# Kernel tuning notes

Measured on AMD Instinct MI355X. Metric: run time of the kernel, lower is better.

The kernel has to match this reference:

```python
import jax, jax.numpy as jnp
import numpy as np

GAMMAS = (0.01, 0.1, 1.0, 10.0, 100.0)
FOCAL_GAMMA = 2.0
SMOOTH = 0.1
TASK_W = (0.4, 0.3, 0.3)
A_RECON, A_ORTH, A_ADV = 1.0, 0.1, 0.1
NUM_DOMAINS = 4
NUM_LABELS1 = 4


def focal_smooth(logits, targets, maskf):
    # FocalLoss.forward with smoothing > 0, masked mean
    n_classes = logits.shape[1]
    log_p = jax.nn.log_softmax(logits, axis=1)
    p = jnp.exp(log_p)
    onehot = jax.nn.one_hot(targets, n_classes, dtype=logits.dtype)
    smooth = onehot * (1.0 - SMOOTH) + SMOOTH / n_classes
    ce = -(smooth * log_p).sum(axis=1)
    pt = jnp.take_along_axis(p, targets[:, None], axis=1)[:, 0]
    loss = ce * (1.0 - pt) ** FOCAL_GAMMA
    return (loss * maskf).sum() / jnp.maximum(maskf.sum(), 1.0)


def ce_masked(logits, targets, maskf):
    log_p = jax.nn.log_softmax(logits, axis=1)
    nll = -jnp.take_along_axis(log_p, targets[:, None], axis=1)[:, 0]
    return (nll * maskf).sum() / jnp.maximum(maskf.sum(), 1.0)


def cond_mmd(feats, domains, labels, maskf):
    # Global pairwise sq-distance matrix; multi-gamma RBF kernels summed.
    sq = (feats ** 2).sum(axis=-1)                      # (B,)
    Dmat = sq[:, None] + sq[None, :] - 2.0 * feats @ feats.T  # (B,B)
    Ksum = jnp.zeros_like(Dmat)
    for g in GAMMAS:
        Ksum = Ksum + jnp.exp(-g * Dmat)
    loss = jnp.asarray(0.0, feats.dtype)
    count = jnp.asarray(0.0, feats.dtype)
    for lab in range(NUM_LABELS1):
        lm = (labels == lab).astype(feats.dtype) * maskf
        for d1 in range(NUM_DOMAINS):
            m1 = lm * (domains == d1).astype(feats.dtype)
            n1 = m1.sum()
            Km1 = Ksum @ m1
            for d2 in range(d1 + 1, NUM_DOMAINS):
                m2 = lm * (domains == d2).astype(feats.dtype)
                n2 = m2.sum()
                valid = (n1 > 1) & (n2 > 1)
                term = (m1 @ Km1) / jnp.maximum(n1, 1.0) ** 2 \
                     + (m2 @ (Ksum @ m2)) / jnp.maximum(n2, 1.0) ** 2 \
                     - 2.0 * (m2 @ Km1) / jnp.maximum(n1 * n2, 1.0)
                loss = loss + jnp.where(valid, term, 0.0)
                count = count + valid.astype(feats.dtype)
    return loss / jnp.maximum(count, 1.0)


def hsic(c, s):
    n = c.shape[0]
    c = c / jnp.maximum(jnp.linalg.norm(c, axis=-1, keepdims=True), 1e-12)
    s = s / jnp.maximum(jnp.linalg.norm(s, axis=-1, keepdims=True), 1e-12)
    K = c @ c.T
    L = s @ s.T
    Kc = K - K.mean(axis=0, keepdims=True) - K.mean(axis=1, keepdims=True) + K.mean()
    Lc = L - L.mean(axis=0, keepdims=True) - L.mean(axis=1, keepdims=True) + L.mean()
    return (Kc * Lc).sum() / (n - 1) ** 2


def setup_inputs() -> dict:
    key = jax.random.key(0)
    ks = jax.random.split(key, 20)
    B, D, H = 4096, 256, 768
    inp = {
        'logits1': jax.random.normal(ks[0], (B, 4), jnp.float32),
        'labels1': jax.random.randint(ks[1], (B,), 0, 4),
        'logits2': jax.random.normal(ks[2], (B, 6), jnp.float32),
        'labels2': jax.random.randint(ks[3], (B,), 0, 6),
        'logits3': jax.random.normal(ks[4], (B, 3), jnp.float32),
        'labels3': jax.random.randint(ks[5], (B,), 0, 3),
        'c_v': jax.random.normal(ks[6], (B, D), jnp.float32),
        's_v': jax.random.normal(ks[7], (B, D), jnp.float32),
        'c_t': jax.random.normal(ks[8], (B, D), jnp.float32),
        's_t': jax.random.normal(ks[9], (B, D), jnp.float32),
        'v_sv': jax.random.normal(ks[10], (B, NUM_DOMAINS), jnp.float32),
        'v_st': jax.random.normal(ks[11], (B, NUM_DOMAINS), jnp.float32),
        'domain_labels': jax.random.randint(ks[12], (B,), 0, NUM_DOMAINS),
        'mask': jnp.ones((B,), dtype=bool),
        'h_img_recon': jax.random.normal(ks[13], (B, H), jnp.float32),
        'h_img_orig': jax.random.normal(ks[14], (B, H), jnp.float32),
        'h_txt_recon': jax.random.normal(ks[15], (B, H), jnp.float32),
        'h_txt_orig': jax.random.normal(ks[16], (B, H), jnp.float32),
    }
    return inp


def reference(logits1, labels1, logits2, labels2, logits3, labels3,
              c_v, s_v, c_t, s_t, v_sv, v_st, domain_labels, mask,
              h_img_recon, h_img_orig, h_txt_recon, h_txt_orig):
    maskf = mask.astype(jnp.float32)
    total = jnp.asarray(0.0, jnp.float32)
    # classification (focal + label smoothing), per-task weighted
    total = total + TASK_W[0] * focal_smooth(logits1, labels1, maskf)
    total = total + TASK_W[1] * focal_smooth(logits2, labels2, maskf)
    total = total + TASK_W[2] * focal_smooth(logits3, labels3, maskf)
    # adversarial: CE on spurious domain logits + conditional MMD on causal feats
    l_adv_s = ce_masked(v_sv, domain_labels, maskf) + ce_masked(v_st, domain_labels, maskf)
    l_adv_c = cond_mmd(c_v, domain_labels, labels1, maskf) \
            + cond_mmd(c_t, domain_labels, labels1, maskf)
    total = total + A_ADV * (l_adv_s + l_adv_c)
    # orthogonality (HSIC), on unmasked features as in source
    l_orth = hsic(c_v, s_v) + hsic(c_t, s_t)
    total = total + A_ORTH * l_orth
    # reconstruction MSE
    l_recon = jnp.mean((h_img_recon - h_img_orig) ** 2) + jnp.mean((h_txt_recon - h_txt_orig) ** 2)
    total = total + A_RECON * l_recon
    return total
```

## Files before the change

### kernel.cpp

```cpp
#include <hip/hip_runtime.h>
#include <hip/hip_bf16.h>


typedef short bf16x8 __attribute__((ext_vector_type(8)));
typedef float f32x4 __attribute__((ext_vector_type(4)));
typedef unsigned long long u64;
typedef unsigned int u32;

static constexpr int D = 256;
static constexpr int H = 768;
static constexpr int NG = 16;
static constexpr float FX32 = 4294967296.f;
static constexpr float IFX32 = 2.3283064365386963e-10f;

__device__ inline void gAddFx(u64* p, float v) {
  long long q = (long long)llroundf(v * FX32);
  atomicAdd(p, (u64)q);
}
__device__ inline float fxToF(u64 v) { return (float)(long long)v * IFX32; }

__device__ inline float focal_n(const float* x, int n, int tgt,
                                float s_over_n, float oms) {
  float mx = x[0];
  for (int c = 1; c < n; ++c) mx = fmaxf(mx, x[c]);
  float se = 0.f, sx = 0.f;
  for (int c = 0; c < n; ++c) { se += __expf(x[c] - mx); sx += x[c]; }
  float logZ = mx + __logf(se);
  float ce = logZ - oms * x[tgt] - s_over_n * sx;
  float pt = __expf(x[tgt] - logZ);
  float om = 1.f - pt;
  return ce * om * om;
}

extern "C" __global__ __launch_bounds__(256) void k_pre(
    const void* __restrict__ mask, const int* __restrict__ y1,
    const int* __restrict__ dom,
    const float* __restrict__ l1, const float* __restrict__ l2,
    const float* __restrict__ l3, const int* __restrict__ y2,
    const int* __restrict__ y3,
    const float* __restrict__ vsv, const float* __restrict__ vst,
    const float* __restrict__ cv, const float* __restrict__ sv,
    const float* __restrict__ ct, const float* __restrict__ st,
    const float* __restrict__ ir, const float* __restrict__ io,
    const float* __restrict__ trc, const float* __restrict__ to,
    u64* SA, u64* GCU, u64* U64,
    int* gid, float* sq, float* inv, unsigned short* bf,
    int B, int N4, int NA, int NB) {
  __shared__ u32 sh3[3];
  __shared__ u32 cnt[NG];
  __shared__ int redi[4];
  __shared__ float redf[4];
  int bid = blockIdx.x;
  int t = threadIdx.x;

  if (bid < NA) {
    if (t < 3) sh3[t] = 0;
    if (t < NG) cnt[t] = 0;
    __syncthreads();
    u32 a = 0, b2 = 0, cd = 0;
    if (t * 16 + 15 < B) {
      uint4 wv = ((const uint4*)mask)[t];
      u32 ws[4] = {wv.x, wv.y, wv.z, wv.w};
      #pragma unroll
      for (int j = 0; j < 4; ++j) {
        a |= ws[j] & 0xffu; b2 |= ws[j] & 0xff00u; cd |= ws[j] & 0xffff0000u;
      }
    }
    if (a) atomicOr(&sh3[0], 1u);
    if (b2) atomicOr(&sh3[1], 1u);
    if (cd) atomicOr(&sh3[2], 1u);
    __syncthreads();
    int mode;
    if ((sh3[1] | sh3[2]) == 0) mode = 0;
    else if (sh3[0] == 0 && sh3[1] == 0) mode = 1;
    else mode = 2;
    int r = bid * 256 + t;
    int mi = 0;
    float s[5] = {0.f, 0.f, 0.f, 0.f, 0.f};
    if (r < B) {
      if (mode == 0)      mi = ((const int*)mask)[r] ? 1 : 0;
      else if (mode == 1) mi = (((const float*)mask)[r] != 0.f) ? 1 : 0;
      else                mi = ((const unsigned char*)mask)[r] ? 1 : 0;
      int g = -1;
      if (mi) { g = y1[r] * 4 + dom[r]; atomicAdd(&cnt[g], 1u); }
      gid[r] = g;
      if (mi) {
        float x[6];
        for (int c = 0; c < 4; ++c) x[c] = l1[r * 4 + c];
        s[0] = focal_n(x, 4, y1[r], 0.1f / 4.f, 0.9f);
        for (int c = 0; c < 6; ++c) x[c] = l2[r * 6 + c];
        s[1] = focal_n(x, 6, y2[r], 0.1f / 6.f, 0.9f);
        for (int c = 0; c < 3; ++c) x[c] = l3[r * 3 + c];
        s[2] = focal_n(x, 3, y3[r], 0.1f / 3.f, 0.9f);
        int d = dom[r];
        for (int c = 0; c < 4; ++c) x[c] = vsv[r * 4 + c];
        {
          float mx = fmaxf(fmaxf(x[0], x[1]), fmaxf(x[2], x[3]));
          float se = __expf(x[0]-mx)+__expf(x[1]-mx)+__expf(x[2]-mx)+__expf(x[3]-mx);
          s[3] = mx + __logf(se) - x[d];
        }
        for (int c = 0; c < 4; ++c) x[c] = vst[r * 4 + c];
        {
          float mx = fmaxf(fmaxf(x[0], x[1]), fmaxf(x[2], x[3]));
          float se = __expf(x[0]-mx)+__expf(x[1]-mx)+__expf(x[2]-mx)+__expf(x[3]-mx);
          s[4] = mx + __logf(se) - x[d];
        }
      }
    }
    int v = mi;
    #pragma unroll
    for (int o = 32; o > 0; o >>= 1) v += __shfl_down(v, o);
    if ((t & 63) == 0) redi[t >> 6] = v;
    __syncthreads();
    if (t == 0) atomicAdd(&SA[5], (u64)(redi[0] + redi[1] + redi[2] + redi[3]));
    if (t < NG && cnt[t]) atomicAdd(&GCU[t], (u64)cnt[t]);
    for (int k = 0; k < 5; ++k) {
      float x = s[k];
      #pragma unroll
      for (int o = 32; o > 0; o >>= 1) x += __shfl_down(x, o);
      __syncthreads();
      if ((t & 63) == 0) redf[t >> 6] = x;
      __syncthreads();
      if (t == 0) gAddFx(&SA[k], redf[0] + redf[1] + redf[2] + redf[3]);
    }
  } else if (bid < NA + NB) {
    int b = bid - NA;
    int f = b >> 6;
    int rb = b & 63;
    const float* p = (f == 0) ? cv : (f == 1) ? sv : (f == 2) ? ct : st;
    int w = t >> 6, L = t & 63;
    float up0 = 0.f, up1 = 0.f, up2 = 0.f, up3 = 0.f;
    for (int k = 0; k < 16; ++k) {
      int r = rb * 64 + w * 16 + k;
      float4 v = ((const float4*)(p + (size_t)r * D))[L];
      float ss = v.x * v.x + v.y * v.y + v.z * v.z + v.w * v.w;
      #pragma unroll
      for (int o = 32; o > 0; o >>= 1) ss += __shfl_down(ss, o);
      ss = __shfl(ss, 0);
      float iv = 1.f / fmaxf(sqrtf(ss), 1e-12f);
      if ((f & 1) == 0) {
        int fi = f >> 1;
        alignas(8) __hip_bfloat16 hb[4];
        hb[0] = __float2bfloat16(v.x); hb[1] = __float2bfloat16(v.y);
        hb[2] = __float2bfloat16(v.z); hb[3] = __float2bfloat16(v.w);
        *(uint2*)(bf + ((size_t)fi * B + r) * D + L * 4) = *(uint2*)hb;
        if (L == 0) sq[fi * B + r] = ss;
      }
      if (L == 0) inv[f * B + r] = iv;
      up0 += v.x * iv; up1 += v.y * iv; up2 += v.z * iv; up3 += v.w * iv;
    }
    u64* Uf = U64 + f * D + 4 * L;
    gAddFx(Uf + 0, up0); gAddFx(Uf + 1, up1);
    gAddFx(Uf + 2, up2); gAddFx(Uf + 3, up3);
  } else {
    int cidx = bid - (NA + NB);
    int j = cidx >> 8;
    int cb = cidx & 255;
    const float4* A  = (const float4*)(j ? trc : ir);
    const float4* Bp = (const float4*)(j ? to : io);
    float acc = 0.f;
    for (int idx = cb * 256 + t; idx < N4; idx += 256 * 256) {
      float4 a = A[idx], b = Bp[idx];
      float dx = a.x-b.x, dy = a.y-b.y, dz = a.z-b.z, dw = a.w-b.w;
      acc += dx*dx + dy*dy + dz*dz + dw*dw;
    }
    #pragma unroll
    for (int o = 32; o > 0; o >>= 1) acc += __shfl_down(acc, o);
    if ((t & 63) == 0) redf[t >> 6] = acc;
    __syncthreads();
    if (t == 0) gAddFx(&SA[6 + j], redf[0] + redf[1] + redf[2] + redf[3]);
  }
}

extern "C" __global__ __launch_bounds__(256) void k_big(
    const float* __restrict__ cv, const float* __restrict__ sv,
    const float* __restrict__ ct, const float* __restrict__ st,
    const float* __restrict__ inv, u64* M64,
    const unsigned short* __restrict__ bf, const float* __restrict__ sq,
    const int* __restrict__ gid, u64* GSP, int B) {
  __shared__ __align__(16) char smem[38016];
  int bid = blockIdx.x;
  int tid = threadIdx.x;

  if (bid < 512) {
    float (*lc)[16] = (float(*)[16])smem;
    float* lis = (float*)(smem + 16384);
    int p = bid >> 8;
    int a0 = ((bid >> 4) & 15) * 16;
    int i0 = (bid & 15) * 256;
    const float* c = p ? ct : cv;
    const float* s = p ? st : sv;
    const float* ic = inv + (2 * p) * B;
    const float* is = inv + (2 * p + 1) * B;
    int t = tid;
    if (t < 256) lis[t] = is[i0 + t];
    for (int e = t; e < 256 * 16; e += 256) {
      int i = e >> 4, rr = e & 15;
      lc[i][rr] = c[(size_t)(i0 + i) * D + a0 + rr] * ic[i0 + i];
    }
    __syncthreads();
    float4 acc[4];
    #pragma unroll
    for (int r = 0; r < 4; ++r) acc[r] = make_float4(0.f, 0.f, 0.f, 0.f);
    #pragma unroll 8
    for (int i = 0; i < 256; ++i) {
      float svv = s[(size_t)(i0 + i) * D + t] * lis[i];
      const float4* lr = (const float4*)lc[i];
      #pragma unroll
      for (int r = 0; r < 4; ++r) {
        float4 c4 = lr[r];
        acc[r].x += c4.x * svv; acc[r].y += c4.y * svv;
        acc[r].z += c4.z * svv; acc[r].w += c4.w * svv;
      }
    }
    u64* Mp = M64 + (size_t)p * D * D;
    #pragma unroll
    for (int r = 0; r < 4; ++r) {
      gAddFx(&Mp[(a0 + 4 * r + 0) * D + t], acc[r].x);
      gAddFx(&Mp[(a0 + 4 * r + 1) * D + t], acc[r].y);
      gAddFx(&Mp[(a0 + 4 * r + 2) * D + t], acc[r].z);
      gAddFx(&Mp[(a0 + 4 * r + 3) * D + t], acc[r].w);
    }
    return;
  }

  unsigned short* Ab = (unsigned short*)smem;
  unsigned short* Bb = (unsigned short*)(smem + 16384);
  u32 (*gsw)[264] = (u32(*)[264])(smem + 32768);
  int*   gA = (int*)(smem + 36992);
  int*   gB = gA + 64;
  float* sA = (float*)(gB + 64);
  float* sB = sA + 64;

  int idx2 = bid - 512;
  int feat = idx2 & 1;
  int tlin = idx2 >> 1;
  int NT = B / 64;
  float tf = (float)tlin;
  int ti = (int)((2.f * NT + 1.f -
                  sqrtf((2.f * NT + 1.f) * (2.f * NT + 1.f) - 8.f * tf)) * 0.5f);
  while (ti > 0 && (ti * NT - (ti * (ti - 1)) / 2) > tlin) --ti;
  while (((ti + 1) * NT - ((ti + 1) * ti) / 2) <= tlin) ++ti;
  int tj = ti + (tlin - (ti * NT - (ti * (ti - 1)) / 2));
  int i0 = ti * 64, j0 = tj * 64;
  bool diag = (ti == tj);
  const unsigned short* fb = bf + (size_t)feat * B * D;
  const float* sqf = sq + (size_t)feat * B;

  int w = tid >> 6, L = tid & 63, m = L & 15, q = L >> 4;

  {
    u32* gz = (u32*)gsw;
    for (int e = tid; e < 4 * 264; e += 256) gz[e] = 0;
    if (tid < 64) { gA[tid] = gid[i0 + tid]; sA[tid] = sqf[i0 + tid]; }
    else if (tid < 128) { int r = tid - 64; gB[r] = gid[j0 + r]; sB[r] = sqf[j0 + r]; }
  }

  f32x4 acc[4] = {{0.f,0.f,0.f,0.f},{0.f,0.f,0.f,0.f},{0.f,0.f,0.f,0.f},{0.f,0.f,0.f,0.f}};

  for (int h = 0; h < 2; ++h) {
    if (h) __syncthreads();
    for (int e = tid; e < 1024; e += 256) {
      int row = e >> 4, ck = e & 15;
      uint4 v = *(const uint4*)(fb + (size_t)(i0 + row) * D + h * 128 + ck * 8);
      *(uint4*)&Ab[row * 128 + ((ck ^ (row & 15)) * 8)] = v;
    }
    if (!diag) {
      for (int e = tid; e < 1024; e += 256) {
        int row = e >> 4, ck = e & 15;
        uint4 v = *(const uint4*)(fb + (size_t)(j0 + row) * D + h * 128 + ck * 8);
        *(uint4*)&Bb[row * 128 + ((ck ^ (row & 15)) * 8)] = v;
      }
    }
    __syncthreads();
    const unsigned short* Bp = diag ? Ab : Bb;
    #pragma unroll
    for (int kk = 0; kk < 4; ++kk) {
      int ar = w * 16 + m;
      bf16x8 aF = *(const bf16x8*)&Ab[ar * 128 + (((kk * 4 + q) ^ (ar & 15)) * 8)];
      #pragma unroll
      for (int c = 0; c < 4; ++c) {
        int br = c * 16 + m;
        bf16x8 bF = *(const bf16x8*)&Bp[br * 128 + (((kk * 4 + q) ^ (br & 15)) * 8)];
        acc[c] = __builtin_amdgcn_mfma_f32_16x16x32_bf16(aF, bF, acc[c], 0, 0, 0);
      }
    }
  }
  int ri0 = w * 16 + q * 4;
  int gi0 = gA[ri0], gi1 = gA[ri0+1], gi2 = gA[ri0+2], gi3 = gA[ri0+3];
  float si0 = sA[ri0], si1 = sA[ri0+1], si2 = sA[ri0+2], si3 = sA[ri0+3];
  int giv[4] = {gi0, gi1, gi2, gi3};
  float siv[4] = {si0, si1, si2, si3};
  #pragma unroll
  for (int c = 0; c < 4; ++c) {
    int rj = c * 16 + m;
    int gj = gB[rj];
    float sb = sB[rj];
    #pragma unroll
    for (int v = 0; v < 4; ++v) {
      int ri = ri0 + v;
      int gi = giv[v];
      if (gi >= 0 && gj >= 0 && !(diag && ri > rj)) {
        float K;
        if (diag && ri == rj) K = 5.f;
        else {
          float d = fmaxf(siv[v] + sb - 2.f * acc[c][v], 0.f);
          K = __expf(-0.01f * d) + __expf(-0.1f * d) + __expf(-d)
            + __expf(-10.f * d) + __expf(-100.f * d);
        }
        u32 kf = (u32)(K * 65536.f + 0.5f);
        int a = min(gi, gj), b = max(gi, gj);
        atomicAdd(&gsw[w][a * NG + b], kf);
      }
    }
  }
  __syncthreads();
  if (tid < NG * NG) {
    u64 s = (u64)gsw[0][tid] + gsw[1][tid] + gsw[2][tid] + gsw[3][tid];
    if (s)
      atomicAdd(&GSP[((size_t)(tlin & 63) * 2 + feat) * NG * NG + tid], s);
  }
}

extern "C" __global__ __launch_bounds__(256) void k_hsic(
    const u64* __restrict__ U64, const u64* __restrict__ M64, u64* SA) {
  __shared__ float red[8];
  __shared__ float ush[32], vsh[D];
  int p = blockIdx.y;
  int k0 = blockIdx.x * 32;
  int t = threadIdx.x;
  vsh[t] = fxToF(U64[(2 * p + 1) * D + t]);
  if (t < 32) ush[t] = fxToF(U64[(2 * p) * D + k0 + t]);
  __syncthreads();
  const u64* Mp = M64 + (size_t)p * D * D;
  float trkl = 0.f, cr = 0.f;
  #pragma unroll 4
  for (int k = 0; k < 32; ++k) {
    float mv = fxToF(Mp[(size_t)(k0 + k) * D + t]);
    trkl += mv * mv;
    cr += ush[k] * mv;
  }
  cr *= vsh[t];
  #pragma unroll
  for (int o = 32; o > 0; o >>= 1) { trkl += __shfl_down(trkl, o); cr += __shfl_down(cr, o); }
  if ((t & 63) == 0) { red[t >> 6] = trkl; red[4 + (t >> 6)] = cr; }
  __syncthreads();
  if (t == 0) gAddFx(&SA[10 + p], red[0] + red[1] + red[2] + red[3]);
  if (t == 64) gAddFx(&SA[12 + p], red[4] + red[5] + red[6] + red[7]);
}

extern "C" __global__ __launch_bounds__(256) void k_final(
    const u64* SA, const u64* GCU, const u64* GSP,
    const u64* U64, float* out, int B) {
  __shared__ float red[8];
  __shared__ float gssh[2 * NG * NG];
  int t = threadIdx.x;
  for (int e = t; e < 2 * NG * NG; e += 256) {
    u64 ssum = 0;
    int f = e >> 8, idx = e & 255;
    for (int cpy = 0; cpy < 64; ++cpy)
      ssum += GSP[((size_t)cpy * 2 + f) * NG * NG + idx];
    gssh[e] = (float)((double)ssum * (1.0 / 65536.0));
  }
  __syncthreads();

  float n = (float)B;
  float hs[2];
  for (int p = 0; p < 2; ++p) {
    float ut = fxToF(U64[(2 * p) * D + t]);
    float vt = fxToF(U64[(2 * p + 1) * D + t]);
    float uu = ut * ut, vv = vt * vt;
    #pragma unroll
    for (int o = 32; o > 0; o >>= 1) { uu += __shfl_down(uu, o); vv += __shfl_down(vv, o); }
    __syncthreads();
    if ((t & 63) == 0) { red[t >> 6] = uu; red[4 + (t >> 6)] = vv; }
    __syncthreads();
    float uus = red[0] + red[1] + red[2] + red[3];
    float vvs = red[4] + red[5] + red[6] + red[7];
    float trkl = (float)((double)(long long)SA[10 + p] * (double)IFX32);
    float cr   = (float)((double)(long long)SA[12 + p] * (double)IFX32);
    hs[p] = (trkl - (2.f / n) * cr + uus * vvs / (n * n))
          / ((n - 1.f) * (n - 1.f));
    __syncthreads();
  }
  if (t == 0) {
    float msum = fmaxf((float)SA[5], 1.f);
    float f1 = fxToF(SA[0]) / msum;
    float f2 = fxToF(SA[1]) / msum;
    float f3 = fxToF(SA[2]) / msum;
    float cesv = fxToF(SA[3]) / msum;
    float cest = fxToF(SA[4]) / msum;
    float mmd[2];
    for (int f = 0; f < 2; ++f) {
      float loss = 0.f, cntv = 0.f;
      for (int lab = 0; lab < 4; ++lab)
        for (int d1 = 0; d1 < 4; ++d1)
          for (int d2 = d1 + 1; d2 < 4; ++d2) {
            int a = lab * 4 + d1, b = lab * 4 + d2;
            float n1 = (float)GCU[a], n2 = (float)GCU[b];
            if (n1 > 1.f && n2 > 1.f) {
              float g11 = 2.f * gssh[f * 256 + a * NG + a] - 5.f * n1;
              float g22 = 2.f * gssh[f * 256 + b * NG + b] - 5.f * n2;
              float g12 = gssh[f * 256 + a * NG + b];
              loss += g11 / (fmaxf(n1, 1.f) * fmaxf(n1, 1.f))
                    + g22 / (fmaxf(n2, 1.f) * fmaxf(n2, 1.f))
                    - 2.f * g12 / fmaxf(n1 * n2, 1.f);
              cntv += 1.f;
            }
          }
      mmd[f] = loss / fmaxf(cntv, 1.f);
    }
    double rs = ((double)(long long)SA[6] + (double)(long long)SA[7])
              * (double)IFX32;
    float recon = (float)(rs / ((double)B * (double)H));
    float total = 0.4f * f1 + 0.3f * f2 + 0.3f * f3
                + 0.1f * (cesv + cest + mmd[0] + mmd[1])
                + 0.1f * (hs[0] + hs[1])
                + recon;
    out[0] = total;
  }
}

extern "C" void kernel_launch(void* const* d_in, const int* in_sizes, int n_in,
                              void* d_out, int out_size, void* d_ws, size_t ws_size,
                              hipStream_t stream) {
  const float* l1  = (const float*)d_in[0];
  const int*   y1  = (const int*)d_in[1];
  const float* l2  = (const float*)d_in[2];
  const int*   y2  = (const int*)d_in[3];
  const float* l3  = (const float*)d_in[4];
  const int*   y3  = (const int*)d_in[5];
  const float* cv  = (const float*)d_in[6];
  const float* sv  = (const float*)d_in[7];
  const float* ct  = (const float*)d_in[8];
  const float* st  = (const float*)d_in[9];
  const float* vsv = (const float*)d_in[10];
  const float* vst = (const float*)d_in[11];
  const int*   dom = (const int*)d_in[12];
  const void*  mask= d_in[13];
  const float* ir  = (const float*)d_in[14];
  const float* io  = (const float*)d_in[15];
  const float* trc = (const float*)d_in[16];
  const float* to  = (const float*)d_in[17];
  int B = in_sizes[1];

  u64* SA  = (u64*)d_ws;
  u64* GCU = SA + 32;
  u64* U64 = GCU + 16;
  u64* M64 = U64 + 4 * D;
  u64* GSP = M64 + 2 * D * D;
  u64* zend = GSP + 64 * 2 * NG * NG;
  size_t zeroBytes = (size_t)((char*)zend - (char*)d_ws);
  int*   gid = (int*)zend;
  float* sq  = (float*)(gid + B);
  float* inv = sq + 2 * B;
  unsigned short* bf = (unsigned short*)(inv + 4 * B);

  int NA = B / 256;
  int NB = 4 * (B / 64);
  int NC = 512;
  int N4 = B * H / 4;

  hipMemsetAsync(d_ws, 0, zeroBytes, stream);
  k_pre<<<NA + NB + NC, 256, 0, stream>>>(
      mask, y1, dom, l1, l2, l3, y2, y3, vsv, vst,
      cv, sv, ct, st, ir, io, trc, to,
      SA, GCU, U64, gid, sq, inv, bf, B, N4, NA, NB);
  int NT = B / 64;
  int nmmd = 2 * (NT * (NT + 1) / 2);
  k_big<<<512 + nmmd, 256, 0, stream>>>(cv, sv, ct, st, inv, M64,
                                        bf, sq, gid, GSP, B);
  k_hsic<<<dim3(8, 2), 256, 0, stream>>>(U64, M64, SA);
  k_final<<<1, 256, 0, stream>>>(SA, GCU, GSP, U64, (float*)d_out, B);
}
```

Measured before the change: 249.4 us.

## Sort rows by label-domain group to replace per-element LDS atomics in MMD tiles

Adds a counting-sort kernel that permutes samples by (label, domain) group, with masked rows placed last. The MMD tiles then gather rows through the permutation. Tiles made only of masked rows exit early, and tiles spanning at most two groups per axis reduce the kernel sums in registers with a wave shuffle and issue a few global atomics, instead of one shared-memory atomic per element. The K-loop is re-tiled to 64-wide chunks, which cuts shared memory and can raise occupancy. In exchange it adds a kernel launch, gathered (non-contiguous) row loads, and a slow fallback path with per-element global atomics for tiles that span many groups.

```diff
diff --git a/kernel.cpp b/kernel.cpp
--- a/kernel.cpp
+++ b/kernel.cpp
@@ -44,10 +44,10 @@
     const float* __restrict__ ir, const float* __restrict__ io,
     const float* __restrict__ trc, const float* __restrict__ to,
     u64* SA, u64* GCU, u64* U64,
-    int* gid, float* sq, float* inv, unsigned short* bf,
+    int* gid, float* sq, float* inv, unsigned short* bf, u32* CNTB,
     int B, int N4, int NA, int NB) {
   __shared__ u32 sh3[3];
-  __shared__ u32 cnt[NG];
+  __shared__ u32 cnt[17];
   __shared__ int redi[4];
   __shared__ float redf[4];
   int bid = blockIdx.x;
@@ -55,7 +55,7 @@
 
   if (bid < NA) {
     if (t < 3) sh3[t] = 0;
-    if (t < NG) cnt[t] = 0;
+    if (t < 17) cnt[t] = 0;
     __syncthreads();
     u32 a = 0, b2 = 0, cd = 0;
     if (t * 16 + 15 < B) {
@@ -83,6 +83,7 @@
       else                mi = ((const unsigned char*)mask)[r] ? 1 : 0;
       int g = -1;
       if (mi) { g = y1[r] * 4 + dom[r]; atomicAdd(&cnt[g], 1u); }
+      else atomicAdd(&cnt[16], 1u);
       gid[r] = g;
       if (mi) {
         float x[6];
@@ -114,6 +115,7 @@
     __syncthreads();
     if (t == 0) atomicAdd(&SA[5], (u64)(redi[0] + redi[1] + redi[2] + redi[3]));
     if (t < NG && cnt[t]) atomicAdd(&GCU[t], (u64)cnt[t]);
+    if (t < 17) CNTB[bid * 17 + t] = cnt[t];
     for (int k = 0; k < 5; ++k) {
       float x = s[k];
       #pragma unroll
@@ -172,13 +174,52 @@
   }
 }
 
+extern "C" __global__ __launch_bounds__(256) void k_sort(
+    const u32* __restrict__ CNTB, const int* __restrict__ gid,
+    const float* __restrict__ sq, int* __restrict__ perm,
+    float* __restrict__ sqp, int* __restrict__ OFF, int B, int NA) {
+  __shared__ int lg[256];
+  __shared__ u32 cbs[17], tots[17];
+  int b = blockIdx.x, t = threadIdx.x;
+  if (t < 17) {
+    u32 cb = 0, tot = 0;
+    for (int b2 = 0; b2 < NA; ++b2) {
+      u32 c = CNTB[b2 * 17 + t];
+      cb += (b2 < b) ? c : 0u;
+      tot += c;
+    }
+    cbs[t] = cb; tots[t] = tot;
+  }
+  int r = b * 256 + t;
+  int g = 16;
+  if (r < B) { int gg = gid[r]; g = (gg < 0) ? 16 : gg; }
+  lg[t] = g;
+  __syncthreads();
+  if (b == 0 && t < 18) {
+    u32 bb = 0;
+    for (int g2 = 0; g2 < t; ++g2) bb += tots[g2];
+    OFF[t] = (int)bb;
+  }
+  if (r < B) {
+    u32 base = 0;
+    for (int g2 = 0; g2 < g; ++g2) base += tots[g2];
+    int rank = 0;
+    for (int t2 = 0; t2 < t; ++t2) rank += (lg[t2] == g) ? 1 : 0;
+    int pos = (int)(base + cbs[g]) + rank;
+    perm[pos] = r;
+    sqp[pos] = sq[r];
+    sqp[B + pos] = sq[B + r];
+  }
+}
+
 extern "C" __global__ __launch_bounds__(256) void k_big(
     const float* __restrict__ cv, const float* __restrict__ sv,
     const float* __restrict__ ct, const float* __restrict__ st,
     const float* __restrict__ inv, u64* M64,
-    const unsigned short* __restrict__ bf, const float* __restrict__ sq,
-    const int* __restrict__ gid, u64* GSP, int B) {
-  __shared__ __align__(16) char smem[38016];
+    const unsigned short* __restrict__ bf, const float* __restrict__ sqp,
+    const int* __restrict__ perm, const int* __restrict__ OFF,
+    u64* GSP, int B) {
+  __shared__ __align__(16) char smem[17536];
   int bid = blockIdx.x;
   int tid = threadIdx.x;
 
@@ -225,12 +266,12 @@
   }
 
   unsigned short* Ab = (unsigned short*)smem;
-  unsigned short* Bb = (unsigned short*)(smem + 16384);
-  u32 (*gsw)[264] = (u32(*)[264])(smem + 32768);
-  int*   gA = (int*)(smem + 36992);
-  int*   gB = gA + 64;
-  float* sA = (float*)(gB + 64);
-  float* sB = sA + 64;
+  unsigned short* Bb = (unsigned short*)(smem + 8192);
+  float* sA = (float*)(smem + 16384);
+  float* sB = (float*)(smem + 16640);
+  int*   pA = (int*)(smem + 16896);
+  int*   pB = (int*)(smem + 17152);
+  int*   offs = (int*)(smem + 17408);
 
   int idx2 = bid - 512;
   int feat = idx2 & 1;
@@ -245,80 +286,146 @@
   int i0 = ti * 64, j0 = tj * 64;
   bool diag = (ti == tj);
   const unsigned short* fb = bf + (size_t)feat * B * D;
-  const float* sqf = sq + (size_t)feat * B;
+  const float* sqf = sqp + (size_t)feat * B;
 
   int w = tid >> 6, L = tid & 63, m = L & 15, q = L >> 4;
 
-  {
-    u32* gz = (u32*)gsw;
-    for (int e = tid; e < 4 * 264; e += 256) gz[e] = 0;
-    if (tid < 64) { gA[tid] = gid[i0 + tid]; sA[tid] = sqf[i0 + tid]; }
-    else if (tid < 128) { int r = tid - 64; gB[r] = gid[j0 + r]; sB[r] = sqf[j0 + r]; }
-  }
-
-  f32x4 acc[4] = {{0.f,0.f,0.f,0.f},{0.f,0.f,0.f,0.f},{0.f,0.f,0.f,0.f},{0.f,0.f,0.f,0.f}};
-
-  for (int h = 0; h < 2; ++h) {
-    if (h) __syncthreads();
-    for (int e = tid; e < 1024; e += 256) {
-      int row = e >> 4, ck = e & 15;
-      uint4 v = *(const uint4*)(fb + (size_t)(i0 + row) * D + h * 128 + ck * 8);
-      *(uint4*)&Ab[row * 128 + ((ck ^ (row & 15)) * 8)] = v;
+  if (tid < 64) { pA[tid] = perm[i0 + tid]; sA[tid] = sqf[i0 + tid]; }
+  else if (tid < 128) { int r = tid - 64; pB[r] = perm[j0 + r]; sB[r] = sqf[j0 + r]; }
+  else if (tid < 146) offs[tid - 128] = OFF[tid - 128];
+  __syncthreads();
+
+  int gr0 = 0, nbr = 0, gc0 = 0, ncb = 0;
+  #pragma unroll
+  for (int g = 1; g <= 17; ++g) {
+    int o = offs[g];
+    gr0 += (o <= i0) ? 1 : 0;
+    nbr += (o > i0 && o < i0 + 64) ? 1 : 0;
+    gc0 += (o <= j0) ? 1 : 0;
+    ncb += (o > j0 && o < j0 + 64) ? 1 : 0;
+  }
+  if (gr0 == 16 || gc0 == 16) return;
+  int gr1 = gr0 + nbr;
+  int gc1 = gc0 + ncb;
+  int s_r = nbr ? offs[gr1] : i0 + 64;
+  int s_c = ncb ? offs[gc1] : j0 + 64;
+
+  f32x4 acc[4] = {{0.f,0.f,0.f,0.f},{0.f,0.f,0.f,0.f},
+                  {0.f,0.f,0.f,0.f},{0.f,0.f,0.f,0.f}};
+
+  for (int hq = 0; hq < 4; ++hq) {
+    if (hq) __syncthreads();
+    for (int e = tid; e < 512; e += 256) {
+      int row = e >> 3, ck = e & 7;
+      uint4 v = *(const uint4*)(fb + (size_t)pA[row] * D + hq * 64 + ck * 8);
+      *(uint4*)&Ab[row * 64 + ((ck ^ (row & 7)) * 8)] = v;
     }
     if (!diag) {
-      for (int e = tid; e < 1024; e += 256) {
-        int row = e >> 4, ck = e & 15;
-        uint4 v = *(const uint4*)(fb + (size_t)(j0 + row) * D + h * 128 + ck * 8);
-        *(uint4*)&Bb[row * 128 + ((ck ^ (row & 15)) * 8)] = v;
+      for (int e = tid; e < 512; e += 256) {
+        int row = e >> 3, ck = e & 7;
+        uint4 v = *(const uint4*)(fb + (size_t)pB[row] * D + hq * 64 + ck * 8);
+        *(uint4*)&Bb[row * 64 + ((ck ^ (row & 7)) * 8)] = v;
       }
     }
     __syncthreads();
     const unsigned short* Bp = diag ? Ab : Bb;
-    #pragma unroll
-    for (int kk = 0; kk < 4; ++kk) {
-      int ar = w * 16 + m;
-      bf16x8 aF = *(const bf16x8*)&Ab[ar * 128 + (((kk * 4 + q) ^ (ar & 15)) * 8)];
+    int ar = w * 16 + m;
+    #pragma unroll
+    for (int kk = 0; kk < 2; ++kk) {
+      bf16x8 aF = *(const bf16x8*)&Ab[ar * 64 + (((kk * 4 + q) ^ (ar & 7)) * 8)];
       #pragma unroll
       for (int c = 0; c < 4; ++c) {
         int br = c * 16 + m;
-        bf16x8 bF = *(const bf16x8*)&Bp[br * 128 + (((kk * 4 + q) ^ (br & 15)) * 8)];
+        bf16x8 bF = *(const bf16x8*)&Bp[br * 64 + (((kk * 4 + q) ^ (br & 7)) * 8)];
         acc[c] = __builtin_amdgcn_mfma_f32_16x16x32_bf16(aF, bF, acc[c], 0, 0, 0);
       }
     }
   }
+
   int ri0 = w * 16 + q * 4;
-  int gi0 = gA[ri0], gi1 = gA[ri0+1], gi2 = gA[ri0+2], gi3 = gA[ri0+3];
-  float si0 = sA[ri0], si1 = sA[ri0+1], si2 = sA[ri0+2], si3 = sA[ri0+3];
-  int giv[4] = {gi0, gi1, gi2, gi3};
-  float siv[4] = {si0, si1, si2, si3};
-  #pragma unroll
-  for (int c = 0; c < 4; ++c) {
-    int rj = c * 16 + m;
-    int gj = gB[rj];
-    float sb = sB[rj];
+  u64* gsp = GSP + ((size_t)(tlin & 63) * 2 + feat) * NG * NG;
+
+  if (nbr <= 1 && ncb <= 1) {
+    float siv[4]; bool rhiv[4];
     #pragma unroll
     for (int v = 0; v < 4; ++v) {
-      int ri = ri0 + v;
-      int gi = giv[v];
-      if (gi >= 0 && gj >= 0 && !(diag && ri > rj)) {
-        float K;
-        if (diag && ri == rj) K = 5.f;
-        else {
-          float d = fmaxf(siv[v] + sb - 2.f * acc[c][v], 0.f);
-          K = __expf(-0.01f * d) + __expf(-0.1f * d) + __expf(-d)
-            + __expf(-10.f * d) + __expf(-100.f * d);
+      siv[v] = sA[ri0 + v];
+      rhiv[v] = (i0 + ri0 + v) >= s_r;
+    }
+    float a00 = 0.f, a01 = 0.f, a10 = 0.f, a11 = 0.f;
+    #pragma unroll
+    for (int c = 0; c < 4; ++c) {
+      int rj = c * 16 + m;
+      float sb = sB[rj];
+      float lo = 0.f, hi = 0.f;
+      #pragma unroll
+      for (int v = 0; v < 4; ++v) {
+        float d = fmaxf(siv[v] + sb - 2.f * acc[c][v], 0.f);
+        float K = __expf(-0.01f * d) + __expf(-0.1f * d) + __expf(-d)
+                + __expf(-10.f * d) + __expf(-100.f * d);
+        if (diag) {
+          int ri = ri0 + v;
+          K = (ri > rj) ? 0.f : (ri == rj) ? 5.f : K;
         }
-        u32 kf = (u32)(K * 65536.f + 0.5f);
-        int a = min(gi, gj), b = max(gi, gj);
-        atomicAdd(&gsw[w][a * NG + b], kf);
-      }
-    }
-  }
-  __syncthreads();
-  if (tid < NG * NG) {
-    u64 s = (u64)gsw[0][tid] + gsw[1][tid] + gsw[2][tid] + gsw[3][tid];
-    if (s)
-      atomicAdd(&GSP[((size_t)(tlin & 63) * 2 + feat) * NG * NG + tid], s);
+        float kh = rhiv[v] ? K : 0.f;
+        hi += kh; lo += K - kh;
+      }
+      bool chi = (j0 + rj) >= s_c;
+      float loH = chi ? lo : 0.f;
+      float hiH = chi ? hi : 0.f;
+      a00 += lo - loH; a01 += loH;
+      a10 += hi - hiH; a11 += hiH;
+    }
+    #pragma unroll
+    for (int o = 32; o > 0; o >>= 1) {
+      a00 += __shfl_down(a00, o); a01 += __shfl_down(a01, o);
+      a10 += __shfl_down(a10, o); a11 += __shfl_down(a11, o);
+    }
+    if (L == 0) {
+      if (a00 != 0.f)
+        atomicAdd(&gsp[gr0 * NG + gc0], (u64)(long long)llroundf(a00 * 65536.f));
+      if (a01 != 0.f && gc1 < 16)
+        atomicAdd(&gsp[gr0 * NG + gc1], (u64)(long long)llroundf(a01 * 65536.f));
+      if (a10 != 0.f && gr1 < 16)
+        atomicAdd(&gsp[gr1 * NG + gc0], (u64)(long long)llroundf(a10 * 65536.f));
+      if (a11 != 0.f && gr1 < 16 && gc1 < 16)
+        atomicAdd(&gsp[gr1 * NG + gc1], (u64)(long long)llroundf(a11 * 65536.f));
+    }
+  } else {
+    int giv[4]; float siv[4];
+    #pragma unroll
+    for (int v = 0; v < 4; ++v) {
+      int idx = i0 + ri0 + v;
+      int g = 0;
+      #pragma unroll
+      for (int k = 1; k <= 16; ++k) g += (offs[k] <= idx) ? 1 : 0;
+      giv[v] = g;
+      siv[v] = sA[ri0 + v];
+    }
+    #pragma unroll
+    for (int c = 0; c < 4; ++c) {
+      int rj = c * 16 + m;
+      int jdx = j0 + rj;
+      int gj = 0;
+      #pragma unroll
+      for (int k = 1; k <= 16; ++k) gj += (offs[k] <= jdx) ? 1 : 0;
+      float sb = sB[rj];
+      #pragma unroll
+      for (int v = 0; v < 4; ++v) {
+        int ri = ri0 + v;
+        if (giv[v] < 16 && gj < 16 && !(diag && ri > rj)) {
+          float K;
+          if (diag && ri == rj) K = 5.f;
+          else {
+            float d = fmaxf(siv[v] + sb - 2.f * acc[c][v], 0.f);
+            K = __expf(-0.01f * d) + __expf(-0.1f * d) + __expf(-d)
+              + __expf(-10.f * d) + __expf(-100.f * d);
+          }
+          u32 kf = (u32)(K * 65536.f + 0.5f);
+          atomicAdd(&gsp[giv[v] * NG + gj], (u64)kf);
+        }
+      }
+    }
   }
 }
 
@@ -455,6 +562,10 @@
   float* sq  = (float*)(gid + B);
   float* inv = sq + 2 * B;
   unsigned short* bf = (unsigned short*)(inv + 4 * B);
+  int*   perm = (int*)(bf + 2 * (size_t)B * D);
+  float* sqp  = (float*)(perm + B);
+  int*   OFF  = (int*)(sqp + 2 * B);
+  u32*   CNTB = (u32*)(OFF + 18);
 
   int NA = B / 256;
   int NB = 4 * (B / 64);
@@ -465,11 +576,12 @@
   k_pre<<<NA + NB + NC, 256, 0, stream>>>(
       mask, y1, dom, l1, l2, l3, y2, y3, vsv, vst,
       cv, sv, ct, st, ir, io, trc, to,
-      SA, GCU, U64, gid, sq, inv, bf, B, N4, NA, NB);
+      SA, GCU, U64, gid, sq, inv, bf, CNTB, B, N4, NA, NB);
+  k_sort<<<NA, 256, 0, stream>>>(CNTB, gid, sq, perm, sqp, OFF, B, NA);
   int NT = B / 64;
   int nmmd = 2 * (NT * (NT + 1) / 2);
   k_big<<<512 + nmmd, 256, 0, stream>>>(cv, sv, ct, st, inv, M64,
-                                        bf, sq, gid, GSP, B);
+                                        bf, sqp, perm, OFF, GSP, B);
   k_hsic<<<dim3(8, 2), 256, 0, stream>>>(U64, M64, SA);
   k_final<<<1, 256, 0, stream>>>(SA, GCU, GSP, U64, (float*)d_out, B);
 }
```

Result: no change. 253.3 us (+1.6%).
